# Performance work log

Hardware: AMD Instinct MI355X
Metric: run time of the kernel (lower is better)

The kernel has to match this reference:

```python
import jax, jax.numpy as jnp
import numpy as np

B, S, ENC, DEC = 32, 4096, 512, 512


def setup_inputs() -> dict:
    key = jax.random.key(0)
    k1, k2, k3, k4, k5 = jax.random.split(key, 5)
    return {
        "decoder_hidden": jax.random.normal(k1, (B, DEC), dtype=jnp.float32),
        "encoder_outputs": jax.random.normal(k2, (B, S, ENC), dtype=jnp.float32),
        "W_attn": jax.random.normal(k3, (DEC, ENC + DEC), dtype=jnp.float32) * (1.0 / np.sqrt(ENC + DEC)),
        "b_attn": jax.random.normal(k4, (DEC,), dtype=jnp.float32) * 0.01,
        "v": jax.random.normal(k5, (DEC,), dtype=jnp.float32) * (1.0 / np.sqrt(DEC)),
    }


def reference(decoder_hidden, encoder_outputs, W_attn, b_attn, v):
    dec_dim = decoder_hidden.shape[-1]
    # torch concatenates (hidden, encoder_outputs) then applies attn;
    # algebraically equivalent split avoids materializing the repeat+concat.
    W_h = W_attn[:, :dec_dim]   # [dec, dec]
    W_e = W_attn[:, dec_dim:]   # [dec, enc]
    # [B, 1, dec] + [B, S, dec] + [dec]
    proj = (jnp.einsum('bd,ed->be', decoder_hidden, W_h)[:, None, :]
            + jnp.einsum('bse,de->bsd', encoder_outputs, W_e)
            + b_attn)
    energy = jnp.tanh(proj)                      # [B, S, dec]
    scores = jnp.einsum('bsd,d->bs', energy, v)  # [B, S]
    return jax.nn.softmax(scores, axis=1)
```

## Files before the change

### kernel.cpp

```cpp
#include <hip/hip_runtime.h>
#include <hip/hip_bf16.h>
#include <stdint.h>


typedef __attribute__((ext_vector_type(8))) short short8;
typedef __attribute__((ext_vector_type(4))) float f32x4;

static __device__ __forceinline__ unsigned short f2bf(float f) {
    union { float f; uint32_t u; } x{f};
    uint32_t u = x.u;
    u += 0x7fffu + ((u >> 16) & 1u);
    return (unsigned short)(u >> 16);
}

static __device__ __forceinline__ float tanh_fast(float x) {
    return 1.0f - 2.0f / (__expf(2.0f * x) + 1.0f);
}

__global__ __launch_bounds__(512) void prep_kernel(
    const float* __restrict__ dh, const float* __restrict__ W_attn,
    const float* __restrict__ b_attn, unsigned short* __restrict__ wsB,
    float* __restrict__ wsP1) {
    __shared__ float dhs[512];
    const int tid = threadIdx.x;
    if (blockIdx.x < 64) {
        int idx = blockIdx.x * 512 + tid;
        int c8 = idx & 7;
        int n  = (idx >> 3) & 511;
        int kt = idx >> 12;
        const float* src = W_attn + (size_t)n * 1024 + 512 + kt * 64 + c8 * 8;
        float4 f0 = *(const float4*)(src);
        float4 f1 = *(const float4*)(src + 4);
        short8 p;
        p[0] = (short)f2bf(f0.x); p[1] = (short)f2bf(f0.y);
        p[2] = (short)f2bf(f0.z); p[3] = (short)f2bf(f0.w);
        p[4] = (short)f2bf(f1.x); p[5] = (short)f2bf(f1.y);
        p[6] = (short)f2bf(f1.z); p[7] = (short)f2bf(f1.w);
        int row = kt * 512 + n;
        int byteInRow = (c8 * 16) ^ ((n & 7) << 4);
        *(short8*)((char*)wsB + (size_t)row * 128 + byteInRow) = p;
    } else {
        int b = blockIdx.x - 64;
        dhs[tid] = dh[b * 512 + tid];
        __syncthreads();
        const float* wrow = W_attn + (size_t)tid * 1024;
        float acc = 0.f;
        #pragma unroll 8
        for (int d = 0; d < 512; d += 4) {
            float4 w = *(const float4*)(wrow + d);
            acc += dhs[d] * w.x + dhs[d + 1] * w.y + dhs[d + 2] * w.z + dhs[d + 3] * w.w;
        }
        wsP1[b * 512 + tid] = acc + b_attn[tid];
    }
}

__global__ __launch_bounds__(512, 2) void fused_kernel(
    const float* __restrict__ enc, const unsigned short* __restrict__ wsB,
    const float* __restrict__ wsP1, const float* __restrict__ vvec,
    float* __restrict__ out) {
    __shared__ char lds[163840];
    char* const Abuf[2] = { lds, lds + 16384 };
    char* const Bbuf[2] = { lds + 32768, lds + 98304 };

    const int tid  = threadIdx.x;
    const int wave = tid >> 6;
    const int lane = tid & 63;
    const int llo  = lane & 15, lhi = lane >> 4;
    const int wr   = wave >> 2, wc = wave & 3;
    const int m0   = blockIdx.x * 128;
    const int b    = m0 >> 12;

    const int ar = tid >> 2, ac = tid & 3;
    const float* aptr = enc + (size_t)(m0 + ar) * 512 + ac * 16;
    const int aoff0 = ar * 128 + (((ac * 32)     ) ^ ((ar & 7) << 4));
    const int aoff1 = ar * 128 + (((ac * 32) + 16) ^ ((ar & 7) << 4));

    f32x4 acc[4][8] = {};
    float4 fa0, fa1, fa2, fa3;

    #define STAGE_A_LOAD(kt)                               \
        do { const float* p_ = aptr + (kt) * 64;           \
             fa0 = *(const float4*)(p_);                   \
             fa1 = *(const float4*)(p_ + 4);               \
             fa2 = *(const float4*)(p_ + 8);               \
             fa3 = *(const float4*)(p_ + 12); } while (0)

    #define STAGE_A_WRITE(Adst)                                          \
        do { short8 p0_, p1_;                                            \
             p0_[0]=(short)f2bf(fa0.x); p0_[1]=(short)f2bf(fa0.y);       \
             p0_[2]=(short)f2bf(fa0.z); p0_[3]=(short)f2bf(fa0.w);       \
             p0_[4]=(short)f2bf(fa1.x); p0_[5]=(short)f2bf(fa1.y);       \
             p0_[6]=(short)f2bf(fa1.z); p0_[7]=(short)f2bf(fa1.w);       \
             p1_[0]=(short)f2bf(fa2.x); p1_[1]=(short)f2bf(fa2.y);       \
             p1_[2]=(short)f2bf(fa2.z); p1_[3]=(short)f2bf(fa2.w);       \
             p1_[4]=(short)f2bf(fa3.x); p1_[5]=(short)f2bf(fa3.y);       \
             p1_[6]=(short)f2bf(fa3.z); p1_[7]=(short)f2bf(fa3.w);       \
             *(short8*)((Adst) + aoff0) = p0_;                           \
             *(short8*)((Adst) + aoff1) = p1_; } while (0)

    #define STAGE_B(kt, Bdst)                                                      \
        do { const char* bsrc_ = (const char*)wsB + (size_t)(kt) * 65536;          \
             _Pragma("unroll")                                                     \
             for (int i_ = 0; i_ < 8; ++i_) {                                      \
                 int off_ = (i_ * 8 + wave) * 1024;                                \
                 __builtin_amdgcn_global_load_lds(                                 \
                     (const uint32_t __attribute__((address_space(1)))*)(bsrc_ + off_ + lane * 16), \
                     (uint32_t __attribute__((address_space(3)))*)((Bdst) + off_), \
                     16, 0, 0);                                                    \
             } } while (0)

    #define COMPUTE(Asrc, Bsrc)                                                    \
        do { _Pragma("unroll")                                                     \
             for (int kk = 0; kk < 2; ++kk) {                                      \
                 const int gbyte = kk * 64 + lhi * 16;                             \
                 short8 af[4], bfr[8];                                             \
                 _Pragma("unroll")                                                 \
                 for (int mi = 0; mi < 4; ++mi) {                                  \
                     int row = wr * 64 + mi * 16 + llo;                            \
                     af[mi] = *(const short8*)((Asrc) + row * 128 +                \
                                               (gbyte ^ ((row & 7) << 4)));        \
                 }                                                                 \
                 _Pragma("unroll")                                                 \
                 for (int ni = 0; ni < 8; ++ni) {                                  \
                     int n = wc * 128 + ni * 16 + llo;                             \
                     bfr[ni] = *(const short8*)((Bsrc) + n * 128 +                 \
                                                (gbyte ^ ((n & 7) << 4)));         \
                 }                                                                 \
                 _Pragma("unroll")                                                 \
                 for (int mi = 0; mi < 4; ++mi)                                    \
                     _Pragma("unroll")                                             \
                     for (int ni = 0; ni < 8; ++ni)                                \
                         acc[mi][ni] = __builtin_amdgcn_mfma_f32_16x16x32_bf16(    \
                             af[mi], bfr[ni], acc[mi][ni], 0, 0, 0);               \
             } } while (0)

    STAGE_A_LOAD(0);
    STAGE_B(0, Bbuf[0]);
    STAGE_A_WRITE(Abuf[0]);
    __syncthreads();

    #pragma unroll
    for (int kt = 0; kt < 8; ++kt) {
        const int cur = kt & 1, nxt = cur ^ 1;
        if (kt < 7) {
            STAGE_A_LOAD(kt + 1);
            STAGE_B(kt + 1, Bbuf[nxt]);
        }
        COMPUTE(Abuf[cur], Bbuf[cur]);
        if (kt < 7) STAGE_A_WRITE(Abuf[nxt]);
        __syncthreads();
    }

    float p1v[8], vv[8];
    #pragma unroll
    for (int ni = 0; ni < 8; ++ni) {
        int d = wc * 128 + ni * 16 + llo;
        p1v[ni] = wsP1[b * 512 + d];
        vv[ni]  = vvec[d];
    }
    float part[16];
    #pragma unroll
    for (int mi = 0; mi < 4; ++mi)
        #pragma unroll
        for (int r = 0; r < 4; ++r) {
            float s = 0.f;
            #pragma unroll
            for (int ni = 0; ni < 8; ++ni)
                s += tanh_fast(acc[mi][ni][r] + p1v[ni]) * vv[ni];
            part[mi * 4 + r] = s;
        }
    #pragma unroll
    for (int off = 1; off < 16; off <<= 1)
        #pragma unroll
        for (int i = 0; i < 16; ++i)
            part[i] += __shfl_xor(part[i], off, 64);

    float* red = (float*)lds;
    if (llo == 0) {
        #pragma unroll
        for (int mi = 0; mi < 4; ++mi)
            #pragma unroll
            for (int r = 0; r < 4; ++r)
                red[wc * 128 + wr * 64 + mi * 16 + lhi * 4 + r] = part[mi * 4 + r];
    }
    __syncthreads();
    if (tid < 128) {
        float s = red[tid] + red[128 + tid] + red[256 + tid] + red[384 + tid];
        out[m0 + tid] = s;
    }
}

__global__ __launch_bounds__(256) void softmax_kernel(float* __restrict__ out) {
    __shared__ float wred[8];
    const int b = blockIdx.x, tid = threadIdx.x;
    float* row = out + (size_t)b * 4096;
    float vals[16];
    float lmax = -1e30f;
    #pragma unroll
    for (int i = 0; i < 16; ++i) {
        vals[i] = row[i * 256 + tid];
        lmax = fmaxf(lmax, vals[i]);
    }
    #pragma unroll
    for (int off = 32; off >= 1; off >>= 1)
        lmax = fmaxf(lmax, __shfl_xor(lmax, off, 64));
    if ((tid & 63) == 0) wred[tid >> 6] = lmax;
    __syncthreads();
    float gmax = fmaxf(fmaxf(wred[0], wred[1]), fmaxf(wred[2], wred[3]));
    float lsum = 0.f;
    #pragma unroll
    for (int i = 0; i < 16; ++i) {
        vals[i] = expf(vals[i] - gmax);
        lsum += vals[i];
    }
    #pragma unroll
    for (int off = 32; off >= 1; off >>= 1)
        lsum += __shfl_xor(lsum, off, 64);
    if ((tid & 63) == 0) wred[4 + (tid >> 6)] = lsum;
    __syncthreads();
    float inv = 1.f / (wred[4] + wred[5] + wred[6] + wred[7]);
    #pragma unroll
    for (int i = 0; i < 16; ++i)
        row[i * 256 + tid] = vals[i] * inv;
}

extern "C" void kernel_launch(void* const* d_in, const int* in_sizes, int n_in,
                              void* d_out, int out_size, void* d_ws, size_t ws_size,
                              hipStream_t stream) {
    const float* dh   = (const float*)d_in[0];
    const float* enc  = (const float*)d_in[1];
    const float* Wat  = (const float*)d_in[2];
    const float* batt = (const float*)d_in[3];
    const float* vvec = (const float*)d_in[4];
    float* out = (float*)d_out;

    unsigned short* wsB = (unsigned short*)d_ws;
    float* wsP1 = (float*)((char*)d_ws + 512 * 512 * 2);

    hipLaunchKernelGGL(prep_kernel, dim3(96), dim3(512), 0, stream,
                       dh, Wat, batt, wsB, wsP1);
    hipLaunchKernelGGL(fused_kernel, dim3(1024), dim3(512), 0, stream,
                       enc, wsB, wsP1, vvec, out);
    hipLaunchKernelGGL(softmax_kernel, dim3(32), dim3(256), 0, stream, out);
}
```

Measured before the change: 162.3 us.

## Split fused GEMM into smaller 64x256 tiles with N-split partial scores

The fused projection+tanh+score kernel now uses 64-row by 256-column tiles with 256 threads, giving 4096 blocks. Each block covers half of the dec dimension and writes partial scores to out or a workspace buffer, and the softmax kernel adds the two halves. Double buffering is dropped in favour of a single 40KB LDS buffer, so more blocks fit per CU, and block IDs are remapped so the two column halves of a row tile run at nearby times. In exchange, each encoder row is read twice (once per column half), fp32 partials go through extra global traffic, and each k-step now needs an extra barrier.

```diff
diff --git a/kernel.cpp b/kernel.cpp
--- a/kernel.cpp
+++ b/kernel.cpp
@@ -54,38 +54,42 @@
     }
 }
 
-__global__ __launch_bounds__(512, 2) void fused_kernel(
+__global__ __launch_bounds__(256, 3) void fused_kernel(
     const float* __restrict__ enc, const unsigned short* __restrict__ wsB,
     const float* __restrict__ wsP1, const float* __restrict__ vvec,
-    float* __restrict__ out) {
-    __shared__ char lds[163840];
-    char* const Abuf[2] = { lds, lds + 16384 };
-    char* const Bbuf[2] = { lds + 32768, lds + 98304 };
+    float* __restrict__ out, float* __restrict__ wsS1) {
+    __shared__ char lds[40960];
+    char* const A_lds = lds;
+    char* const B_lds = lds + 8192;
 
     const int tid  = threadIdx.x;
-    const int wave = tid >> 6;
+    const int wc   = tid >> 6;
     const int lane = tid & 63;
     const int llo  = lane & 15, lhi = lane >> 4;
-    const int wr   = wave >> 2, wc = wave & 3;
-    const int m0   = blockIdx.x * 128;
-    const int b    = m0 >> 12;
+
+    const int bid = blockIdx.x;
+    const int lb  = (bid & 7) * 512 + (bid >> 3);
+    const int rb  = lb >> 1, cb = lb & 1;
+    const int m0  = rb * 64;
+    const int b   = m0 >> 12;
 
     const int ar = tid >> 2, ac = tid & 3;
     const float* aptr = enc + (size_t)(m0 + ar) * 512 + ac * 16;
     const int aoff0 = ar * 128 + (((ac * 32)     ) ^ ((ar & 7) << 4));
     const int aoff1 = ar * 128 + (((ac * 32) + 16) ^ ((ar & 7) << 4));
-
-    f32x4 acc[4][8] = {};
+    const char* bbase = (const char*)wsB + cb * 32768;
+
+    f32x4 acc[4][4] = {};
     float4 fa0, fa1, fa2, fa3;
 
-    #define STAGE_A_LOAD(kt)                               \
-        do { const float* p_ = aptr + (kt) * 64;           \
-             fa0 = *(const float4*)(p_);                   \
-             fa1 = *(const float4*)(p_ + 4);               \
-             fa2 = *(const float4*)(p_ + 8);               \
+    #define A_LOAD(kt)                                 \
+        do { const float* p_ = aptr + (kt) * 64;       \
+             fa0 = *(const float4*)(p_);               \
+             fa1 = *(const float4*)(p_ + 4);           \
+             fa2 = *(const float4*)(p_ + 8);           \
              fa3 = *(const float4*)(p_ + 12); } while (0)
 
-    #define STAGE_A_WRITE(Adst)                                          \
+    #define A_WRITE()                                                    \
         do { short8 p0_, p1_;                                            \
              p0_[0]=(short)f2bf(fa0.x); p0_[1]=(short)f2bf(fa0.y);       \
              p0_[2]=(short)f2bf(fa0.z); p0_[3]=(short)f2bf(fa0.w);       \
@@ -95,66 +99,66 @@
              p1_[2]=(short)f2bf(fa2.z); p1_[3]=(short)f2bf(fa2.w);       \
              p1_[4]=(short)f2bf(fa3.x); p1_[5]=(short)f2bf(fa3.y);       \
              p1_[6]=(short)f2bf(fa3.z); p1_[7]=(short)f2bf(fa3.w);       \
-             *(short8*)((Adst) + aoff0) = p0_;                           \
-             *(short8*)((Adst) + aoff1) = p1_; } while (0)
-
-    #define STAGE_B(kt, Bdst)                                                      \
-        do { const char* bsrc_ = (const char*)wsB + (size_t)(kt) * 65536;          \
+             *(short8*)(A_lds + aoff0) = p0_;                            \
+             *(short8*)(A_lds + aoff1) = p1_; } while (0)
+
+    #define B_GLDS(kt)                                                             \
+        do { const char* bsrc_ = bbase + (size_t)(kt) * 65536;                     \
              _Pragma("unroll")                                                     \
              for (int i_ = 0; i_ < 8; ++i_) {                                      \
-                 int off_ = (i_ * 8 + wave) * 1024;                                \
+                 int off_ = i_ * 4096 + wc * 1024;                                 \
                  __builtin_amdgcn_global_load_lds(                                 \
                      (const uint32_t __attribute__((address_space(1)))*)(bsrc_ + off_ + lane * 16), \
-                     (uint32_t __attribute__((address_space(3)))*)((Bdst) + off_), \
+                     (uint32_t __attribute__((address_space(3)))*)(B_lds + off_),  \
                      16, 0, 0);                                                    \
              } } while (0)
 
-    #define COMPUTE(Asrc, Bsrc)                                                    \
+    #define COMPUTE()                                                              \
         do { _Pragma("unroll")                                                     \
              for (int kk = 0; kk < 2; ++kk) {                                      \
                  const int gbyte = kk * 64 + lhi * 16;                             \
-                 short8 af[4], bfr[8];                                             \
+                 short8 af[4], bfr[4];                                             \
                  _Pragma("unroll")                                                 \
                  for (int mi = 0; mi < 4; ++mi) {                                  \
-                     int row = wr * 64 + mi * 16 + llo;                            \
-                     af[mi] = *(const short8*)((Asrc) + row * 128 +                \
+                     int row = mi * 16 + llo;                                      \
+                     af[mi] = *(const short8*)(A_lds + row * 128 +                 \
                                                (gbyte ^ ((row & 7) << 4)));        \
                  }                                                                 \
                  _Pragma("unroll")                                                 \
-                 for (int ni = 0; ni < 8; ++ni) {                                  \
-                     int n = wc * 128 + ni * 16 + llo;                             \
-                     bfr[ni] = *(const short8*)((Bsrc) + n * 128 +                 \
+                 for (int ni = 0; ni < 4; ++ni) {                                  \
+                     int n = wc * 64 + ni * 16 + llo;                              \
+                     bfr[ni] = *(const short8*)(B_lds + n * 128 +                  \
                                                 (gbyte ^ ((n & 7) << 4)));         \
                  }                                                                 \
                  _Pragma("unroll")                                                 \
                  for (int mi = 0; mi < 4; ++mi)                                    \
                      _Pragma("unroll")                                             \
-                     for (int ni = 0; ni < 8; ++ni)                                \
+                     for (int ni = 0; ni < 4; ++ni)                                \
                          acc[mi][ni] = __builtin_amdgcn_mfma_f32_16x16x32_bf16(    \
                              af[mi], bfr[ni], acc[mi][ni], 0, 0, 0);               \
              } } while (0)
 
-    STAGE_A_LOAD(0);
-    STAGE_B(0, Bbuf[0]);
-    STAGE_A_WRITE(Abuf[0]);
+    A_LOAD(0);
+    A_WRITE();
+    B_GLDS(0);
     __syncthreads();
 
     #pragma unroll
     for (int kt = 0; kt < 8; ++kt) {
-        const int cur = kt & 1, nxt = cur ^ 1;
+        if (kt < 7) A_LOAD(kt + 1);
+        COMPUTE();
+        __syncthreads();
         if (kt < 7) {
-            STAGE_A_LOAD(kt + 1);
-            STAGE_B(kt + 1, Bbuf[nxt]);
+            A_WRITE();
+            B_GLDS(kt + 1);
+            __syncthreads();
         }
-        COMPUTE(Abuf[cur], Bbuf[cur]);
-        if (kt < 7) STAGE_A_WRITE(Abuf[nxt]);
-        __syncthreads();
-    }
-
-    float p1v[8], vv[8];
-    #pragma unroll
-    for (int ni = 0; ni < 8; ++ni) {
-        int d = wc * 128 + ni * 16 + llo;
+    }
+
+    float p1v[4], vv[4];
+    #pragma unroll
+    for (int ni = 0; ni < 4; ++ni) {
+        int d = cb * 256 + wc * 64 + ni * 16 + llo;
         p1v[ni] = wsP1[b * 512 + d];
         vv[ni]  = vvec[d];
     }
@@ -165,7 +169,7 @@
         for (int r = 0; r < 4; ++r) {
             float s = 0.f;
             #pragma unroll
-            for (int ni = 0; ni < 8; ++ni)
+            for (int ni = 0; ni < 4; ++ni)
                 s += tanh_fast(acc[mi][ni][r] + p1v[ni]) * vv[ni];
             part[mi * 4 + r] = s;
         }
@@ -181,24 +185,26 @@
         for (int mi = 0; mi < 4; ++mi)
             #pragma unroll
             for (int r = 0; r < 4; ++r)
-                red[wc * 128 + wr * 64 + mi * 16 + lhi * 4 + r] = part[mi * 4 + r];
-    }
-    __syncthreads();
-    if (tid < 128) {
-        float s = red[tid] + red[128 + tid] + red[256 + tid] + red[384 + tid];
-        out[m0 + tid] = s;
-    }
-}
-
-__global__ __launch_bounds__(256) void softmax_kernel(float* __restrict__ out) {
+                red[wc * 64 + mi * 16 + lhi * 4 + r] = part[mi * 4 + r];
+    }
+    __syncthreads();
+    if (tid < 64) {
+        float s = red[tid] + red[64 + tid] + red[128 + tid] + red[192 + tid];
+        (cb ? wsS1 : out)[m0 + tid] = s;
+    }
+}
+
+__global__ __launch_bounds__(256) void softmax_kernel(
+    float* __restrict__ out, const float* __restrict__ wsS1) {
     __shared__ float wred[8];
     const int b = blockIdx.x, tid = threadIdx.x;
     float* row = out + (size_t)b * 4096;
+    const float* row1 = wsS1 + (size_t)b * 4096;
     float vals[16];
     float lmax = -1e30f;
     #pragma unroll
     for (int i = 0; i < 16; ++i) {
-        vals[i] = row[i * 256 + tid];
+        vals[i] = row[i * 256 + tid] + row1[i * 256 + tid];
         lmax = fmaxf(lmax, vals[i]);
     }
     #pragma unroll
@@ -235,11 +241,12 @@
     float* out = (float*)d_out;
 
     unsigned short* wsB = (unsigned short*)d_ws;
-    float* wsP1 = (float*)((char*)d_ws + 512 * 512 * 2);
+    float* wsP1 = (float*)((char*)d_ws + 524288);
+    float* wsS1 = (float*)((char*)d_ws + 589824);
 
     hipLaunchKernelGGL(prep_kernel, dim3(96), dim3(512), 0, stream,
                        dh, Wat, batt, wsB, wsP1);
-    hipLaunchKernelGGL(fused_kernel, dim3(1024), dim3(512), 0, stream,
-                       enc, wsB, wsP1, vvec, out);
-    hipLaunchKernelGGL(softmax_kernel, dim3(32), dim3(256), 0, stream, out);
-}
+    hipLaunchKernelGGL(fused_kernel, dim3(4096), dim3(256), 0, stream,
+                       enc, wsB, wsP1, vvec, out, wsS1);
+    hipLaunchKernelGGL(softmax_kernel, dim3(32), dim3(256), 0, stream, out, wsS1);
+}
```

Measured after the change: 145.3 us. 1.12x faster.

## Deepen GEMM prefetch pipeline with manual waitcnt and remap block order

Applied to the files above, without the earlier changes.

Rewrites the K loop of the fused kernel as a hand-scheduled pipeline that keeps loads for two K-steps in flight. It uses explicit s_waitcnt counts, sched_barrier and raw s_barrier in place of __syncthreads, aiming to overlap global loads of encoder rows and B tiles with MFMA compute. It also permutes the block-to-tile mapping so consecutive block IDs are spread across batches, which may change how L2 and memory channels are used. The hand-set vmcnt values are fragile: if the counts are wrong, a read can race a load, and removing compiler freedom can hurt scheduling. A dead ITER_MAIN macro is left in.

```diff
diff --git a/kernel.cpp b/kernel.cpp
--- a/kernel.cpp
+++ b/kernel.cpp
@@ -59,16 +59,21 @@
     const float* __restrict__ wsP1, const float* __restrict__ vvec,
     float* __restrict__ out) {
     __shared__ char lds[163840];
-    char* const Abuf[2] = { lds, lds + 16384 };
-    char* const Bbuf[2] = { lds + 32768, lds + 98304 };
+    char* const Ab0 = lds;
+    char* const Ab1 = lds + 16384;
+    char* const Bb0 = lds + 32768;
+    char* const Bb1 = lds + 98304;
 
     const int tid  = threadIdx.x;
     const int wave = tid >> 6;
     const int lane = tid & 63;
     const int llo  = lane & 15, lhi = lane >> 4;
     const int wr   = wave >> 2, wc = wave & 3;
-    const int m0   = blockIdx.x * 128;
-    const int b    = m0 >> 12;
+
+    const int bid = blockIdx.x;
+    const int lb  = (bid & 7) * 128 + (bid >> 3);
+    const int m0  = lb * 128;
+    const int b   = m0 >> 12;
 
     const int ar = tid >> 2, ac = tid & 3;
     const float* aptr = enc + (size_t)(m0 + ar) * 512 + ac * 16;
@@ -78,14 +83,18 @@
     f32x4 acc[4][8] = {};
     float4 fa0, fa1, fa2, fa3;
 
-    #define STAGE_A_LOAD(kt)                               \
-        do { const float* p_ = aptr + (kt) * 64;           \
-             fa0 = *(const float4*)(p_);                   \
-             fa1 = *(const float4*)(p_ + 4);               \
-             fa2 = *(const float4*)(p_ + 8);               \
+    #define FENCE() asm volatile("" ::: "memory")
+    #define SCHEDB() __builtin_amdgcn_sched_barrier(0)
+    #define BAR() __builtin_amdgcn_s_barrier()
+
+    #define A_LOAD(kt)                                 \
+        do { const float* p_ = aptr + (kt) * 64;       \
+             fa0 = *(const float4*)(p_);               \
+             fa1 = *(const float4*)(p_ + 4);           \
+             fa2 = *(const float4*)(p_ + 8);           \
              fa3 = *(const float4*)(p_ + 12); } while (0)
 
-    #define STAGE_A_WRITE(Adst)                                          \
+    #define A_WRITE(Adst)                                                \
         do { short8 p0_, p1_;                                            \
              p0_[0]=(short)f2bf(fa0.x); p0_[1]=(short)f2bf(fa0.y);       \
              p0_[2]=(short)f2bf(fa0.z); p0_[3]=(short)f2bf(fa0.w);       \
@@ -98,7 +107,7 @@
              *(short8*)((Adst) + aoff0) = p0_;                           \
              *(short8*)((Adst) + aoff1) = p1_; } while (0)
 
-    #define STAGE_B(kt, Bdst)                                                      \
+    #define B_GLDS(kt, Bdst)                                                       \
         do { const char* bsrc_ = (const char*)wsB + (size_t)(kt) * 65536;          \
              _Pragma("unroll")                                                     \
              for (int i_ = 0; i_ < 8; ++i_) {                                      \
@@ -134,22 +143,59 @@
                              af[mi], bfr[ni], acc[mi][ni], 0, 0, 0);               \
              } } while (0)
 
-    STAGE_A_LOAD(0);
-    STAGE_B(0, Bbuf[0]);
-    STAGE_A_WRITE(Abuf[0]);
-    __syncthreads();
-
-    #pragma unroll
-    for (int kt = 0; kt < 8; ++kt) {
-        const int cur = kt & 1, nxt = cur ^ 1;
-        if (kt < 7) {
-            STAGE_A_LOAD(kt + 1);
-            STAGE_B(kt + 1, Bbuf[nxt]);
-        }
-        COMPUTE(Abuf[cur], Bbuf[cur]);
-        if (kt < 7) STAGE_A_WRITE(Abuf[nxt]);
-        __syncthreads();
-    }
+    A_LOAD(0);
+    FENCE();
+    B_GLDS(0, Bb0);
+    asm volatile("s_waitcnt vmcnt(8)" ::: "memory");
+    SCHEDB();
+    A_WRITE(Ab0);
+    FENCE();
+    A_LOAD(1);
+    FENCE();
+    B_GLDS(1, Bb1);
+    asm volatile("s_waitcnt vmcnt(12) lgkmcnt(0)" ::: "memory");
+    SCHEDB(); BAR(); SCHEDB();
+
+    #define ITER_MAIN(K, AcurS, AnxtS, BcurS, BnxtS)                               \
+        do {                                                                       \
+            asm volatile("s_waitcnt vmcnt(8)" ::: "memory");    \
+            SCHEDB();                                                              \
+            COMPUTE(AcurS, BcurS);                                                 \
+            A_WRITE(AnxtS);                        \
+            SCHEDB(); BAR(); SCHEDB();             \
+            A_LOAD((K) + 2);                                           \
+            FENCE();                                                               \
+            B_GLDS((K) + 2, BcurS == Ab0 ? Bb0 : Bb0);            \
+        } while (0)
+
+    #undef ITER_MAIN
+
+    #define ITER(K, Acur, Anxt, Bcur, Bnxt, DO_ISSUE, WTAIL)                       \
+        do {                                                                       \
+            asm volatile("s_waitcnt vmcnt(8)" ::: "memory");    \
+            SCHEDB();                                                              \
+            COMPUTE(Acur, Bcur);                                                   \
+            A_WRITE(Anxt);                                                         \
+            SCHEDB(); BAR(); SCHEDB();            \
+            if (DO_ISSUE) {                                                        \
+                A_LOAD((K) + 2);                      \
+                FENCE();                                                           \
+                B_GLDS((K) + 2, Bcur);                    \
+            }                                                                      \
+            asm volatile(WTAIL ::: "memory");          \
+            SCHEDB(); BAR(); SCHEDB();         \
+        } while (0)
+
+    ITER(0, Ab0, Ab1, Bb0, Bb1, 1, "s_waitcnt vmcnt(12) lgkmcnt(0)");
+    ITER(1, Ab1, Ab0, Bb1, Bb0, 1, "s_waitcnt vmcnt(12) lgkmcnt(0)");
+    ITER(2, Ab0, Ab1, Bb0, Bb1, 1, "s_waitcnt vmcnt(12) lgkmcnt(0)");
+    ITER(3, Ab1, Ab0, Bb1, Bb0, 1, "s_waitcnt vmcnt(12) lgkmcnt(0)");
+    ITER(4, Ab0, Ab1, Bb0, Bb1, 1, "s_waitcnt vmcnt(12) lgkmcnt(0)");
+    ITER(5, Ab1, Ab0, Bb1, Bb0, 1, "s_waitcnt vmcnt(12) lgkmcnt(0)");
+    ITER(6, Ab0, Ab1, Bb0, Bb1, 0, "s_waitcnt vmcnt(0) lgkmcnt(0)");
+    COMPUTE(Ab1, Bb1);
+
+    __syncthreads();
 
     float p1v[8], vv[8];
     #pragma unroll
@@ -235,7 +281,7 @@
     float* out = (float*)d_out;
 
     unsigned short* wsB = (unsigned short*)d_ws;
-    float* wsP1 = (float*)((char*)d_ws + 512 * 512 * 2);
+    float* wsP1 = (float*)((char*)d_ws + 524288);
 
     hipLaunchKernelGGL(prep_kernel, dim3(96), dim3(512), 0, stream,
                        dh, Wat, batt, wsB, wsP1);
```

Measured after the change: 167.4 us. 1.03x slower.
